# Kernel tuning notes

Hardware: AMD Instinct MI355X
Metric: run time of the kernel (lower is better)

## Reference

```python
import jax, jax.numpy as jnp
import numpy as np

N = 100000      # num_nodes
E = 3200000     # num_edges (avg degree 32)
DIN, DH, DOUT = 128, 128, 64
S, L = 3, 3     # num_scales, num_layers
EPS = 1e-5


def setup_inputs() -> dict:
    key = jax.random.key(0)
    ks = jax.random.split(key, 12)
    sc = 0.05
    x = jax.random.normal(ks[0], (N, DIN), jnp.float32)
    edge_index = jax.random.randint(ks[1], (2, E), 0, N, jnp.int32)
    return {
        'x': x,
        'edge_index': edge_index,
        'W0': jax.random.normal(ks[2], (S, DIN, DH), jnp.float32) * sc,
        'b0': jnp.zeros((S, DH), jnp.float32),
        'W1': jax.random.normal(ks[3], (S, DH, DH), jnp.float32) * sc,
        'b1': jnp.zeros((S, DH), jnp.float32),
        'W2': jax.random.normal(ks[4], (S, DH, DOUT), jnp.float32) * sc,
        'b2': jnp.zeros((S, DOUT), jnp.float32),
        'gamma': jnp.ones((S * L, DH), jnp.float32),   # layer_norms (only first L-1 per scale used)
        'beta': jnp.zeros((S * L, DH), jnp.float32),
        'Wf': jax.random.normal(ks[5], (S * DOUT, DOUT), jnp.float32) * sc,
        'bf': jnp.zeros((DOUT,), jnp.float32),
    }


def _layer_norm(h, g, b):
    mu = jnp.mean(h, axis=-1, keepdims=True)
    var = jnp.mean(jnp.square(h - mu), axis=-1, keepdims=True)
    return (h - mu) * jax.lax.rsqrt(var + EPS) * g + b


def _gcn(h, W, b, src, dst, dis):
    # GCNConv: D^{-1/2}(A+I)D^{-1/2} h W + b  (self-loops handled separately)
    hw = h @ W
    msg = hw[src] * (dis[src] * dis[dst])[:, None]          # gather + edge-scale
    agg = jax.ops.segment_sum(msg, dst, num_segments=N)     # scatter-add
    agg = agg + hw * (dis * dis)[:, None]                   # self-loop term
    return agg + b


def reference(x, edge_index, W0, b0, W1, b1, W2, b2, gamma, beta, Wf, bf):
    src, dst = edge_index[0], edge_index[1]
    # degree on A + I (unit edge weights + self loop)
    deg = jax.ops.segment_sum(jnp.ones((E,), x.dtype), dst, num_segments=N) + 1.0
    dis = jax.lax.rsqrt(deg)

    scale_outputs = []
    for s in range(S):
        h = _gcn(x, W0[s], b0[s], src, dst, dis)
        h = _layer_norm(jax.nn.relu(h), gamma[s * L + 0], beta[s * L + 0])  # dropout=identity (eval)
        h = _gcn(h, W1[s], b1[s], src, dst, dis)
        h = _layer_norm(jax.nn.relu(h), gamma[s * L + 1], beta[s * L + 1])
        h = _gcn(h, W2[s], b2[s], src, dst, dis)
        scale_outputs.append(h)

    fused = jnp.concatenate(scale_outputs, axis=-1)  # [N, S*DOUT]
    return fused @ Wf + bf
```

## Files before the change

### kernel.cpp

```cpp
#include <hip/hip_runtime.h>

#define DIN 128
#define DH 128
#define DOUTC 64
#define NS 3
#define NL 3
#define EPSV 1e-5f

typedef __attribute__((ext_vector_type(8))) short bf16x8;
typedef __attribute__((ext_vector_type(4))) float f32x4;

static __device__ inline float bf2f(unsigned short h) {
    unsigned int u = ((unsigned int)h) << 16;
    return __builtin_bit_cast(float, u);
}
static __device__ inline unsigned short f2bf(float f) {
    unsigned int u = __builtin_bit_cast(unsigned int, f);
    u += 0x7fffu + ((u >> 16) & 1u);
    return (unsigned short)(u >> 16);
}
static __device__ inline float lo16(unsigned int u) {
    return __builtin_bit_cast(float, u << 16);
}
static __device__ inline float hi16(unsigned int u) {
    return __builtin_bit_cast(float, u & 0xffff0000u);
}

__global__ __launch_bounds__(256) void k_count_r(const int* __restrict__ dst,
                                                 int* __restrict__ counts, int e, int n) {
    int rg = blockIdx.x & 7;
    int lo = rg * (n >> 3);
    int hi = (rg == 7) ? n : lo + (n >> 3);
    int nb = gridDim.x >> 3, bi = blockIdx.x >> 3;
    for (int i = bi * 256 + threadIdx.x; i < e; i += nb * 256) {
        int d = dst[i];
        if (d >= lo && d < hi) atomicAdd(&counts[d], 1);
    }
}

__global__ void k_dis(const int* __restrict__ counts, float* __restrict__ dis, int n) {
    int i = blockIdx.x * blockDim.x + threadIdx.x;
    if (i < n) dis[i] = rsqrtf((float)counts[i] + 1.0f);
}

__global__ void k_scanA(const int* __restrict__ counts, int* __restrict__ row_start,
                        int* __restrict__ bsums, int n) {
    __shared__ int s[512];
    int t = threadIdx.x;
    int i = blockIdx.x * 512 + t;
    int v = (i < n) ? counts[i] : 0;
    s[t] = v;
    __syncthreads();
    for (int off = 1; off < 512; off <<= 1) {
        int x = s[t];
        if (t >= off) x += s[t - off];
        __syncthreads();
        s[t] = x;
        __syncthreads();
    }
    if (i < n) row_start[i] = s[t] - v;
    if (t == 511) bsums[blockIdx.x] = s[511];
}

__global__ void k_scanB(int* __restrict__ bsums, int nb) {
    __shared__ int s[256];
    int t = threadIdx.x;
    int v = (t < nb) ? bsums[t] : 0;
    s[t] = v;
    __syncthreads();
    for (int off = 1; off < 256; off <<= 1) {
        int x = s[t];
        if (t >= off) x += s[t - off];
        __syncthreads();
        s[t] = x;
        __syncthreads();
    }
    if (t < nb) bsums[t] = s[t] - v;
}

__global__ void k_scanC(int* __restrict__ row_start, const int* __restrict__ bsums, int n) {
    int i = blockIdx.x * blockDim.x + threadIdx.x;
    if (i < n) row_start[i] += bsums[i >> 9];
}

__global__ __launch_bounds__(256) void k_fill_r(const int* __restrict__ src,
                                                const int* __restrict__ dst,
                                                const int* __restrict__ row_start,
                                                int* __restrict__ cursor,
                                                int* __restrict__ col, int e, int n) {
    int rg = blockIdx.x & 7;
    int lo = rg * (n >> 3);
    int hi = (rg == 7) ? n : lo + (n >> 3);
    int nb = gridDim.x >> 3, bi = blockIdx.x >> 3;
    for (int i = bi * 256 + threadIdx.x; i < e; i += nb * 256) {
        int d = dst[i];
        int s = src[i];
        if (d >= lo && d < hi) {
            int p = atomicAdd(&cursor[d], 1);
            col[row_start[d] + p] = s;
        }
    }
}

__global__ void k_prep_w(const float* __restrict__ W0, const float* __restrict__ W1,
                         const float* __restrict__ W2, const float* __restrict__ Wf,
                         const float* __restrict__ b2, const float* __restrict__ bf,
                         unsigned short* __restrict__ Wt0hi, unsigned short* __restrict__ Wt0lo,
                         unsigned short* __restrict__ Wt1hi, unsigned short* __restrict__ Wt1lo,
                         unsigned short* __restrict__ Mhi, unsigned short* __restrict__ Mlo,
                         float* __restrict__ bcomb) {
    int idx = blockIdx.x * blockDim.x + threadIdx.x;
    if (idx < NS * DH * DH) {
        int s = idx / (DH * DH);
        int rem = idx % (DH * DH);
        int o = rem / DH, i = rem % DH;
        {
            float v = W0[(size_t)s * DH * DH + (size_t)i * DH + o];
            unsigned short h = f2bf(v);
            Wt0hi[idx] = h;
            Wt0lo[idx] = f2bf(v - bf2f(h));
        }
        {
            float v = W1[(size_t)s * DH * DH + (size_t)i * DH + o];
            unsigned short h = f2bf(v);
            Wt1hi[idx] = h;
            Wt1lo[idx] = f2bf(v - bf2f(h));
        }
    }
    if (idx < DOUTC * NS * DH) {
        int o = idx / (NS * DH);
        int k = idx % (NS * DH);
        int s = k / DH, i = k % DH;
        float acc = 0.f;
        for (int c = 0; c < DOUTC; ++c)
            acc += W2[((size_t)s * DH + i) * DOUTC + c] * Wf[((size_t)s * DOUTC + c) * DOUTC + o];
        unsigned short h = f2bf(acc);
        Mhi[idx] = h;
        Mlo[idx] = f2bf(acc - bf2f(h));
    }
    if (idx < DOUTC) {
        float acc = bf[idx];
        for (int s = 0; s < NS; ++s)
            for (int c = 0; c < DOUTC; ++c)
                acc += b2[s * DOUTC + c] * Wf[((size_t)s * DOUTC + c) * DOUTC + idx];
        bcomb[idx] = acc;
    }
}

__global__ void k_cvt(const float2* __restrict__ x, unsigned int* __restrict__ xb, int m) {
    int i = blockIdx.x * blockDim.x + threadIdx.x;
    int stride = gridDim.x * blockDim.x;
    for (; i < m; i += stride) {
        float2 v = x[i];
        xb[i] = ((unsigned int)f2bf(v.y) << 16) | f2bf(v.x);
    }
}

__global__ __launch_bounds__(256) void k_agg128(
        const unsigned int* __restrict__ in, unsigned int* __restrict__ out,
        const float* __restrict__ dis, const int* __restrict__ rowstart,
        const int* __restrict__ counts, const int* __restrict__ col, int n) {
    int wid = (blockIdx.x * blockDim.x + threadIdx.x) >> 6;
    int lane = threadIdx.x & 63;
    int nw = (gridDim.x * blockDim.x) >> 6;
    for (int v = wid; v < n; v += nw) {
        float dv = dis[v];
        int st = rowstart[v], cnt = counts[v];
        float a0 = 0.f, a1 = 0.f;
        int i = 0;
        for (; i + 4 <= cnt; i += 4) {
            int s0 = col[st + i], s1 = col[st + i + 1], s2 = col[st + i + 2], s3 = col[st + i + 3];
            float w0 = dis[s0], w1 = dis[s1], w2 = dis[s2], w3 = dis[s3];
            unsigned int u0 = in[(size_t)s0 * 64 + lane];
            unsigned int u1 = in[(size_t)s1 * 64 + lane];
            unsigned int u2 = in[(size_t)s2 * 64 + lane];
            unsigned int u3 = in[(size_t)s3 * 64 + lane];
            a0 += w0 * lo16(u0); a1 += w0 * hi16(u0);
            a0 += w1 * lo16(u1); a1 += w1 * hi16(u1);
            a0 += w2 * lo16(u2); a1 += w2 * hi16(u2);
            a0 += w3 * lo16(u3); a1 += w3 * hi16(u3);
        }
        for (; i < cnt; ++i) {
            int s0 = col[st + i];
            float w0 = dis[s0];
            unsigned int u0 = in[(size_t)s0 * 64 + lane];
            a0 += w0 * lo16(u0); a1 += w0 * hi16(u0);
        }
        unsigned int us = in[(size_t)v * 64 + lane];
        float o0 = dv * (a0 + dv * lo16(us));
        float o1 = dv * (a1 + dv * hi16(us));
        out[(size_t)v * 64 + lane] = ((unsigned int)f2bf(o1) << 16) | f2bf(o0);
    }
}

__global__ __launch_bounds__(256) void k_agg384(
        const unsigned int* __restrict__ in, unsigned int* __restrict__ out,
        const float* __restrict__ dis, const int* __restrict__ rowstart,
        const int* __restrict__ counts, const int* __restrict__ col, int n) {
    int wid = (blockIdx.x * blockDim.x + threadIdx.x) >> 6;
    int lane = threadIdx.x & 63;
    int nw = (gridDim.x * blockDim.x) >> 6;
    for (int v = wid; v < n; v += nw) {
        float dv = dis[v];
        int st = rowstart[v], cnt = counts[v];
        float a0 = 0.f, a1 = 0.f, a2 = 0.f, a3 = 0.f, a4 = 0.f, a5 = 0.f;
        int i = 0;
        for (; i + 2 <= cnt; i += 2) {
            int s0 = col[st + i], s1 = col[st + i + 1];
            float w0 = dis[s0], w1 = dis[s1];
            const unsigned int* p0 = in + (size_t)s0 * 192;
            const unsigned int* p1 = in + (size_t)s1 * 192;
            unsigned int u00 = p0[lane], u01 = p0[lane + 64], u02 = p0[lane + 128];
            unsigned int u10 = p1[lane], u11 = p1[lane + 64], u12 = p1[lane + 128];
            a0 += w0 * lo16(u00); a1 += w0 * hi16(u00);
            a2 += w0 * lo16(u01); a3 += w0 * hi16(u01);
            a4 += w0 * lo16(u02); a5 += w0 * hi16(u02);
            a0 += w1 * lo16(u10); a1 += w1 * hi16(u10);
            a2 += w1 * lo16(u11); a3 += w1 * hi16(u11);
            a4 += w1 * lo16(u12); a5 += w1 * hi16(u12);
        }
        for (; i < cnt; ++i) {
            int s0 = col[st + i];
            float w0 = dis[s0];
            const unsigned int* p0 = in + (size_t)s0 * 192;
            unsigned int u00 = p0[lane], u01 = p0[lane + 64], u02 = p0[lane + 128];
            a0 += w0 * lo16(u00); a1 += w0 * hi16(u00);
            a2 += w0 * lo16(u01); a3 += w0 * hi16(u01);
            a4 += w0 * lo16(u02); a5 += w0 * hi16(u02);
        }
        const unsigned int* ps = in + (size_t)v * 192;
        unsigned int us0 = ps[lane], us1 = ps[lane + 64], us2 = ps[lane + 128];
        float o0 = dv * (a0 + dv * lo16(us0));
        float o1 = dv * (a1 + dv * hi16(us0));
        float o2 = dv * (a2 + dv * lo16(us1));
        float o3 = dv * (a3 + dv * hi16(us1));
        float o4 = dv * (a4 + dv * lo16(us2));
        float o5 = dv * (a5 + dv * hi16(us2));
        unsigned int* po = out + (size_t)v * 192;
        po[lane]       = ((unsigned int)f2bf(o1) << 16) | f2bf(o0);
        po[lane + 64]  = ((unsigned int)f2bf(o3) << 16) | f2bf(o2);
        po[lane + 128] = ((unsigned int)f2bf(o5) << 16) | f2bf(o4);
    }
}

__global__ __launch_bounds__(256) void k_agg64(
        const unsigned int* __restrict__ in, float* __restrict__ out,
        const float* __restrict__ bcomb, const float* __restrict__ dis,
        const int* __restrict__ rowstart, const int* __restrict__ counts,
        const int* __restrict__ col, int n) {
    int wid = (blockIdx.x * blockDim.x + threadIdx.x) >> 6;
    int lane = threadIdx.x & 63;
    int half = lane >> 5, c = lane & 31;
    int nw = (gridDim.x * blockDim.x) >> 6;
    float bc0 = bcomb[c * 2], bc1 = bcomb[c * 2 + 1];
    for (int w = wid; w * 2 < n; w += nw) {
        int v = w * 2 + half;
        if (v >= n) continue;
        float dv = dis[v];
        int st = rowstart[v], cnt = counts[v];
        float a0 = 0.f, a1 = 0.f;
        int i = 0;
        for (; i + 4 <= cnt; i += 4) {
            int s0 = col[st + i], s1 = col[st + i + 1], s2 = col[st + i + 2], s3 = col[st + i + 3];
            float w0 = dis[s0], w1 = dis[s1], w2 = dis[s2], w3 = dis[s3];
            unsigned int u0 = in[(size_t)s0 * 32 + c];
            unsigned int u1 = in[(size_t)s1 * 32 + c];
            unsigned int u2 = in[(size_t)s2 * 32 + c];
            unsigned int u3 = in[(size_t)s3 * 32 + c];
            a0 += w0 * lo16(u0); a1 += w0 * hi16(u0);
            a0 += w1 * lo16(u1); a1 += w1 * hi16(u1);
            a0 += w2 * lo16(u2); a1 += w2 * hi16(u2);
            a0 += w3 * lo16(u3); a1 += w3 * hi16(u3);
        }
        for (; i < cnt; ++i) {
            int s0 = col[st + i];
            float w0 = dis[s0];
            unsigned int u0 = in[(size_t)s0 * 32 + c];
            a0 += w0 * lo16(u0); a1 += w0 * hi16(u0);
        }
        unsigned int us = in[(size_t)v * 32 + c];
        float o0 = dv * (a0 + dv * lo16(us)) + bc0;
        float o1 = dv * (a1 + dv * hi16(us)) + bc1;
        float2 o = make_float2(o0, o1);
        *(float2*)&out[(size_t)v * 64 + c * 2] = o;
    }
}

__global__ __launch_bounds__(256) void k_gemm0(
        const unsigned short* __restrict__ A, const unsigned short* __restrict__ Whi,
        const unsigned short* __restrict__ Wlo, const float* __restrict__ bias,
        const float* __restrict__ gamma, const float* __restrict__ beta,
        unsigned short* __restrict__ out, int n) {
    int wave = threadIdx.x >> 6, lane = threadIdx.x & 63;
    int g = blockIdx.x * 4 + wave;
    if (g * 16 >= n) return;
    int r16 = lane & 15, g4 = lane >> 4;
    int row = g * 16 + r16;
    if (row >= n) row = n - 1;

    bf16x8 a[4];
    #pragma unroll
    for (int ks = 0; ks < 4; ++ks)
        a[ks] = *(const bf16x8*)&A[(size_t)row * DH + ks * 32 + g4 * 8];

    for (int s = 0; s < NS; ++s) {
        const unsigned short* whi = Whi + (size_t)s * DH * DH;
        const unsigned short* wlo = Wlo + (size_t)s * DH * DH;
        f32x4 acc[8];
        #pragma unroll
        for (int t = 0; t < 8; ++t) acc[t] = (f32x4){0.f, 0.f, 0.f, 0.f};
        #pragma unroll
        for (int ks = 0; ks < 4; ++ks) {
            #pragma unroll
            for (int t = 0; t < 8; ++t) {
                size_t wofs = (size_t)(t * 16 + r16) * DH + ks * 32 + g4 * 8;
                bf16x8 bh = *(const bf16x8*)&whi[wofs];
                bf16x8 bl = *(const bf16x8*)&wlo[wofs];
                acc[t] = __builtin_amdgcn_mfma_f32_16x16x32_bf16(a[ks], bh, acc[t], 0, 0, 0);
                acc[t] = __builtin_amdgcn_mfma_f32_16x16x32_bf16(a[ks], bl, acc[t], 0, 0, 0);
            }
        }
        float bia[8], gam[8], bet[8];
        #pragma unroll
        for (int t = 0; t < 8; ++t) {
            bia[t] = bias[s * DH + t * 16 + r16];
            gam[t] = gamma[(size_t)(s * NL + 0) * DH + t * 16 + r16];
            bet[t] = beta[(size_t)(s * NL + 0) * DH + t * 16 + r16];
        }
        #pragma unroll
        for (int r = 0; r < 4; ++r) {
            float y[8];
            float sm = 0.f, q = 0.f;
            #pragma unroll
            for (int t = 0; t < 8; ++t) {
                y[t] = fmaxf(acc[t][r] + bia[t], 0.f);
                sm += y[t];
                q += y[t] * y[t];
            }
            #pragma unroll
            for (int off = 8; off; off >>= 1) {
                sm += __shfl_xor(sm, off);
                q += __shfl_xor(q, off);
            }
            float mu = sm * (1.f / 128.f);
            float var = q * (1.f / 128.f) - mu * mu;
            float rstd = rsqrtf(var + EPSV);
            int node = g * 16 + g4 * 4 + r;
            if (node < n) {
                #pragma unroll
                for (int t = 0; t < 8; ++t) {
                    float o = (y[t] - mu) * rstd * gam[t] + bet[t];
                    out[(size_t)node * (NS * DH) + s * DH + t * 16 + r16] = f2bf(o);
                }
            }
        }
    }
}

__global__ __launch_bounds__(256) void k_gemm1q(
        const unsigned short* __restrict__ G, const unsigned short* __restrict__ Whi,
        const unsigned short* __restrict__ Wlo, const unsigned short* __restrict__ Mhi,
        const unsigned short* __restrict__ Mlo, const float* __restrict__ bias,
        const float* __restrict__ gamma, const float* __restrict__ beta,
        unsigned short* __restrict__ q, int n) {
    __shared__ __align__(16) unsigned short sH[4][16][392];
    int wave = threadIdx.x >> 6, lane = threadIdx.x & 63;
    int g = blockIdx.x * 4 + wave;
    if (g * 16 >= n) return;
    int r16 = lane & 15, g4 = lane >> 4;
    int row = g * 16 + r16;
    if (row >= n) row = n - 1;

    for (int s = 0; s < NS; ++s) {
        bf16x8 a[4];
        #pragma unroll
        for (int ks = 0; ks < 4; ++ks)
            a[ks] = *(const bf16x8*)&G[(size_t)row * (NS * DH) + s * DH + ks * 32 + g4 * 8];
        const unsigned short* whi = Whi + (size_t)s * DH * DH;
        const unsigned short* wlo = Wlo + (size_t)s * DH * DH;
        f32x4 acc[8];
        #pragma unroll
        for (int t = 0; t < 8; ++t) acc[t] = (f32x4){0.f, 0.f, 0.f, 0.f};
        #pragma unroll
        for (int ks = 0; ks < 4; ++ks) {
            #pragma unroll
            for (int t = 0; t < 8; ++t) {
                size_t wofs = (size_t)(t * 16 + r16) * DH + ks * 32 + g4 * 8;
                bf16x8 bh = *(const bf16x8*)&whi[wofs];
                bf16x8 bl = *(const bf16x8*)&wlo[wofs];
                acc[t] = __builtin_amdgcn_mfma_f32_16x16x32_bf16(a[ks], bh, acc[t], 0, 0, 0);
                acc[t] = __builtin_amdgcn_mfma_f32_16x16x32_bf16(a[ks], bl, acc[t], 0, 0, 0);
            }
        }
        float bia[8], gam[8], bet[8];
        #pragma unroll
        for (int t = 0; t < 8; ++t) {
            bia[t] = bias[s * DH + t * 16 + r16];
            gam[t] = gamma[(size_t)(s * NL + 1) * DH + t * 16 + r16];
            bet[t] = beta[(size_t)(s * NL + 1) * DH + t * 16 + r16];
        }
        #pragma unroll
        for (int r = 0; r < 4; ++r) {
            float y[8];
            float sm = 0.f, qq = 0.f;
            #pragma unroll
            for (int t = 0; t < 8; ++t) {
                y[t] = fmaxf(acc[t][r] + bia[t], 0.f);
                sm += y[t];
                qq += y[t] * y[t];
            }
            #pragma unroll
            for (int off = 8; off; off >>= 1) {
                sm += __shfl_xor(sm, off);
                qq += __shfl_xor(qq, off);
            }
            float mu = sm * (1.f / 128.f);
            float var = qq * (1.f / 128.f) - mu * mu;
            float rstd = rsqrtf(var + EPSV);
            #pragma unroll
            for (int t = 0; t < 8; ++t) {
                float o = (y[t] - mu) * rstd * gam[t] + bet[t];
                sH[wave][g4 * 4 + r][s * DH + t * 16 + r16] = f2bf(o);
            }
        }
    }
    __syncthreads();
    f32x4 qa[4];
    #pragma unroll
    for (int t = 0; t < 4; ++t) qa[t] = (f32x4){0.f, 0.f, 0.f, 0.f};
    #pragma unroll
    for (int ks = 0; ks < 12; ++ks) {
        bf16x8 av = *(const bf16x8*)&sH[wave][r16][ks * 32 + g4 * 8];
        #pragma unroll
        for (int t = 0; t < 4; ++t) {
            size_t wofs = (size_t)(t * 16 + r16) * (NS * DH) + ks * 32 + g4 * 8;
            bf16x8 bh = *(const bf16x8*)&Mhi[wofs];
            bf16x8 bl = *(const bf16x8*)&Mlo[wofs];
            qa[t] = __builtin_amdgcn_mfma_f32_16x16x32_bf16(av, bh, qa[t], 0, 0, 0);
            qa[t] = __builtin_amdgcn_mfma_f32_16x16x32_bf16(av, bl, qa[t], 0, 0, 0);
        }
    }
    #pragma unroll
    for (int r = 0; r < 4; ++r) {
        int node = g * 16 + g4 * 4 + r;
        if (node < n) {
            #pragma unroll
            for (int t = 0; t < 4; ++t)
                q[(size_t)node * DOUTC + t * 16 + r16] = f2bf(qa[t][r]);
        }
    }
}

extern "C" void kernel_launch(void* const* d_in, const int* in_sizes, int n_in,
                              void* d_out, int out_size, void* d_ws, size_t ws_size,
                              hipStream_t stream) {
    const float* x    = (const float*)d_in[0];
    const int*   ei   = (const int*)d_in[1];
    const float* W0   = (const float*)d_in[2];
    const float* b0   = (const float*)d_in[3];
    const float* W1   = (const float*)d_in[4];
    const float* b1   = (const float*)d_in[5];
    const float* W2   = (const float*)d_in[6];
    const float* b2   = (const float*)d_in[7];
    const float* gamma= (const float*)d_in[8];
    const float* beta = (const float*)d_in[9];
    const float* Wf   = (const float*)d_in[10];
    const float* bf   = (const float*)d_in[11];
    float* out = (float*)d_out;

    const int n = in_sizes[0] / DIN;
    const int e = in_sizes[1] / 2;
    const int* src = ei;
    const int* dst = ei + e;

    char* ws = (char*)d_ws;
    auto alloc = [&](size_t bytes) {
        char* p = ws;
        ws += (bytes + 255) & ~(size_t)255;
        return p;
    };
    int*   counts   = (int*)alloc((size_t)n * 4);
    int*   cursor   = (int*)alloc((size_t)n * 4);
    int*   rowstart = (int*)alloc((size_t)n * 4);
    int*   bsums    = (int*)alloc(4096);
    float* dis      = (float*)alloc((size_t)n * 4);
    int*   col      = (int*)alloc((size_t)e * 4);
    unsigned short* Wt0hi = (unsigned short*)alloc((size_t)NS * DH * DH * 2);
    unsigned short* Wt0lo = (unsigned short*)alloc((size_t)NS * DH * DH * 2);
    unsigned short* Wt1hi = (unsigned short*)alloc((size_t)NS * DH * DH * 2);
    unsigned short* Wt1lo = (unsigned short*)alloc((size_t)NS * DH * DH * 2);
    unsigned short* Mhi   = (unsigned short*)alloc((size_t)DOUTC * NS * DH * 2);
    unsigned short* Mlo   = (unsigned short*)alloc((size_t)DOUTC * NS * DH * 2);
    float* bcomb    = (float*)alloc(DOUTC * 4);
    unsigned short* xb    = (unsigned short*)alloc((size_t)n * DIN * 2);
    unsigned short* z0    = (unsigned short*)alloc((size_t)n * DH * 2);
    unsigned short* h1cat = (unsigned short*)alloc((size_t)n * NS * DH * 2);
    unsigned short* g1cat = (unsigned short*)alloc((size_t)n * NS * DH * 2);
    unsigned short* q     = (unsigned short*)alloc((size_t)n * DOUTC * 2);

    hipMemsetAsync(counts, 0, (size_t)n * 4, stream);
    hipMemsetAsync(cursor, 0, (size_t)n * 4, stream);

    k_count_r<<<2048, 256, 0, stream>>>(dst, counts, e, n);
    k_dis<<<(n + 255) / 256, 256, 0, stream>>>(counts, dis, n);

    int nb = (n + 511) / 512;
    k_scanA<<<nb, 512, 0, stream>>>(counts, rowstart, bsums, n);
    k_scanB<<<1, 256, 0, stream>>>(bsums, nb);
    k_scanC<<<(n + 255) / 256, 256, 0, stream>>>(rowstart, bsums, n);
    k_fill_r<<<2048, 256, 0, stream>>>(src, dst, rowstart, cursor, col, e, n);

    k_prep_w<<<(NS * DH * DH + 255) / 256, 256, 0, stream>>>(
        W0, W1, W2, Wf, b2, bf, Wt0hi, Wt0lo, Wt1hi, Wt1lo, Mhi, Mlo, bcomb);
    k_cvt<<<2048, 256, 0, stream>>>((const float2*)x, (unsigned int*)xb, n * DIN / 2);

    k_agg128<<<1280, 256, 0, stream>>>((const unsigned int*)xb, (unsigned int*)z0,
                                       dis, rowstart, counts, col, n);
    const int GG = (n / 16 + 3) / 4;
    k_gemm0<<<GG, 256, 0, stream>>>(z0, Wt0hi, Wt0lo, b0, gamma, beta, h1cat, n);
    k_agg384<<<1280, 256, 0, stream>>>((const unsigned int*)h1cat, (unsigned int*)g1cat,
                                       dis, rowstart, counts, col, n);
    k_gemm1q<<<GG, 256, 0, stream>>>(g1cat, Wt1hi, Wt1lo, Mhi, Mlo,
                                     b1, gamma, beta, q, n);
    k_agg64<<<1280, 256, 0, stream>>>((const unsigned int*)q, out, bcomb,
                                      dis, rowstart, counts, col, n);
}
```

Baseline: 1.506 ms.

## Pre-scale features by source norm, vectorize CSR build, tweak aggregation grids

The producer kernels (conversion, gemm0 epilogue, gemm1q epilogue) now multiply each node's row by dis[node]. This removes the per-edge dis[src] gather and multiply from all three aggregation kernels, leaving only a final scale by dis[dst]. Count and fill kernels read dst/src as int4, and cursor is initialised by copying rowstart, so fill writes col directly at the atomic result without a separate row_start read. Aggregation grids grow from 1280 to 2048 blocks and agg384 unrolls by four edges. Rounding changes a little because bf16 values are now stored pre-scaled.

```diff
diff --git a/kernel.cpp b/kernel.cpp
--- a/kernel.cpp
+++ b/kernel.cpp
@@ -32,8 +32,17 @@
     int lo = rg * (n >> 3);
     int hi = (rg == 7) ? n : lo + (n >> 3);
     int nb = gridDim.x >> 3, bi = blockIdx.x >> 3;
-    for (int i = bi * 256 + threadIdx.x; i < e; i += nb * 256) {
-        int d = dst[i];
+    int e4 = e >> 2;
+    const int4* dst4 = (const int4*)dst;
+    for (int i = bi * 256 + threadIdx.x; i < e4; i += nb * 256) {
+        int4 d = dst4[i];
+        if (d.x >= lo && d.x < hi) atomicAdd(&counts[d.x], 1);
+        if (d.y >= lo && d.y < hi) atomicAdd(&counts[d.y], 1);
+        if (d.z >= lo && d.z < hi) atomicAdd(&counts[d.z], 1);
+        if (d.w >= lo && d.w < hi) atomicAdd(&counts[d.w], 1);
+    }
+    if (bi == 0 && (int)threadIdx.x < (e & 3)) {
+        int d = dst[e4 * 4 + threadIdx.x];
         if (d >= lo && d < hi) atomicAdd(&counts[d], 1);
     }
 }
@@ -85,20 +94,27 @@
 
 __global__ __launch_bounds__(256) void k_fill_r(const int* __restrict__ src,
                                                 const int* __restrict__ dst,
-                                                const int* __restrict__ row_start,
                                                 int* __restrict__ cursor,
                                                 int* __restrict__ col, int e, int n) {
     int rg = blockIdx.x & 7;
     int lo = rg * (n >> 3);
     int hi = (rg == 7) ? n : lo + (n >> 3);
     int nb = gridDim.x >> 3, bi = blockIdx.x >> 3;
-    for (int i = bi * 256 + threadIdx.x; i < e; i += nb * 256) {
-        int d = dst[i];
-        int s = src[i];
-        if (d >= lo && d < hi) {
-            int p = atomicAdd(&cursor[d], 1);
-            col[row_start[d] + p] = s;
-        }
+    int e4 = e >> 2;
+    const int4* dst4 = (const int4*)dst;
+    const int4* src4 = (const int4*)src;
+    for (int i = bi * 256 + threadIdx.x; i < e4; i += nb * 256) {
+        int4 d = dst4[i];
+        int4 s = src4[i];
+        if (d.x >= lo && d.x < hi) col[atomicAdd(&cursor[d.x], 1)] = s.x;
+        if (d.y >= lo && d.y < hi) col[atomicAdd(&cursor[d.y], 1)] = s.y;
+        if (d.z >= lo && d.z < hi) col[atomicAdd(&cursor[d.z], 1)] = s.z;
+        if (d.w >= lo && d.w < hi) col[atomicAdd(&cursor[d.w], 1)] = s.w;
+    }
+    if (bi == 0 && (int)threadIdx.x < (e & 3)) {
+        int d = dst[e4 * 4 + threadIdx.x];
+        int s = src[e4 * 4 + threadIdx.x];
+        if (d >= lo && d < hi) col[atomicAdd(&cursor[d], 1)] = s;
     }
 }
 
@@ -147,12 +163,14 @@
     }
 }
 
-__global__ void k_cvt(const float2* __restrict__ x, unsigned int* __restrict__ xb, int m) {
+__global__ void k_cvt(const float2* __restrict__ x, unsigned int* __restrict__ xb,
+                      const float* __restrict__ dis, int m) {
     int i = blockIdx.x * blockDim.x + threadIdx.x;
     int stride = gridDim.x * blockDim.x;
     for (; i < m; i += stride) {
+        float d = dis[i >> 6];
         float2 v = x[i];
-        xb[i] = ((unsigned int)f2bf(v.y) << 16) | f2bf(v.x);
+        xb[i] = ((unsigned int)f2bf(v.y * d) << 16) | f2bf(v.x * d);
     }
 }
 
@@ -165,31 +183,27 @@
     int nw = (gridDim.x * blockDim.x) >> 6;
     for (int v = wid; v < n; v += nw) {
         float dv = dis[v];
-        int st = rowstart[v], cnt = counts[v];
-        float a0 = 0.f, a1 = 0.f;
+        const int* colp = col + rowstart[v];
+        int cnt = counts[v];
+        unsigned int us = in[(size_t)v * 64 + lane];
+        float a0 = lo16(us), a1 = hi16(us);
         int i = 0;
         for (; i + 4 <= cnt; i += 4) {
-            int s0 = col[st + i], s1 = col[st + i + 1], s2 = col[st + i + 2], s3 = col[st + i + 3];
-            float w0 = dis[s0], w1 = dis[s1], w2 = dis[s2], w3 = dis[s3];
+            int s0 = colp[i], s1 = colp[i + 1], s2 = colp[i + 2], s3 = colp[i + 3];
             unsigned int u0 = in[(size_t)s0 * 64 + lane];
             unsigned int u1 = in[(size_t)s1 * 64 + lane];
             unsigned int u2 = in[(size_t)s2 * 64 + lane];
             unsigned int u3 = in[(size_t)s3 * 64 + lane];
-            a0 += w0 * lo16(u0); a1 += w0 * hi16(u0);
-            a0 += w1 * lo16(u1); a1 += w1 * hi16(u1);
-            a0 += w2 * lo16(u2); a1 += w2 * hi16(u2);
-            a0 += w3 * lo16(u3); a1 += w3 * hi16(u3);
+            a0 += lo16(u0); a1 += hi16(u0);
+            a0 += lo16(u1); a1 += hi16(u1);
+            a0 += lo16(u2); a1 += hi16(u2);
+            a0 += lo16(u3); a1 += hi16(u3);
         }
         for (; i < cnt; ++i) {
-            int s0 = col[st + i];
-            float w0 = dis[s0];
-            unsigned int u0 = in[(size_t)s0 * 64 + lane];
-            a0 += w0 * lo16(u0); a1 += w0 * hi16(u0);
-        }
-        unsigned int us = in[(size_t)v * 64 + lane];
-        float o0 = dv * (a0 + dv * lo16(us));
-        float o1 = dv * (a1 + dv * hi16(us));
-        out[(size_t)v * 64 + lane] = ((unsigned int)f2bf(o1) << 16) | f2bf(o0);
+            unsigned int u0 = in[(size_t)colp[i] * 64 + lane];
+            a0 += lo16(u0); a1 += hi16(u0);
+        }
+        out[(size_t)v * 64 + lane] = ((unsigned int)f2bf(dv * a1) << 16) | f2bf(dv * a0);
     }
 }
 
@@ -202,44 +216,48 @@
     int nw = (gridDim.x * blockDim.x) >> 6;
     for (int v = wid; v < n; v += nw) {
         float dv = dis[v];
-        int st = rowstart[v], cnt = counts[v];
-        float a0 = 0.f, a1 = 0.f, a2 = 0.f, a3 = 0.f, a4 = 0.f, a5 = 0.f;
+        const int* colp = col + rowstart[v];
+        int cnt = counts[v];
+        const unsigned int* ps = in + (size_t)v * 192;
+        unsigned int us0 = ps[lane], us1 = ps[lane + 64], us2 = ps[lane + 128];
+        float a0 = lo16(us0), a1 = hi16(us0);
+        float a2 = lo16(us1), a3 = hi16(us1);
+        float a4 = lo16(us2), a5 = hi16(us2);
         int i = 0;
-        for (; i + 2 <= cnt; i += 2) {
-            int s0 = col[st + i], s1 = col[st + i + 1];
-            float w0 = dis[s0], w1 = dis[s1];
+        for (; i + 4 <= cnt; i += 4) {
+            int s0 = colp[i], s1 = colp[i + 1], s2 = colp[i + 2], s3 = colp[i + 3];
             const unsigned int* p0 = in + (size_t)s0 * 192;
             const unsigned int* p1 = in + (size_t)s1 * 192;
+            const unsigned int* p2 = in + (size_t)s2 * 192;
+            const unsigned int* p3 = in + (size_t)s3 * 192;
             unsigned int u00 = p0[lane], u01 = p0[lane + 64], u02 = p0[lane + 128];
             unsigned int u10 = p1[lane], u11 = p1[lane + 64], u12 = p1[lane + 128];
-            a0 += w0 * lo16(u00); a1 += w0 * hi16(u00);
-            a2 += w0 * lo16(u01); a3 += w0 * hi16(u01);
-            a4 += w0 * lo16(u02); a5 += w0 * hi16(u02);
-            a0 += w1 * lo16(u10); a1 += w1 * hi16(u10);
-            a2 += w1 * lo16(u11); a3 += w1 * hi16(u11);
-            a4 += w1 * lo16(u12); a5 += w1 * hi16(u12);
+            unsigned int u20 = p2[lane], u21 = p2[lane + 64], u22 = p2[lane + 128];
+            unsigned int u30 = p3[lane], u31 = p3[lane + 64], u32 = p3[lane + 128];
+            a0 += lo16(u00); a1 += hi16(u00);
+            a2 += lo16(u01); a3 += hi16(u01);
+            a4 += lo16(u02); a5 += hi16(u02);
+            a0 += lo16(u10); a1 += hi16(u10);
+            a2 += lo16(u11); a3 += hi16(u11);
+            a4 += lo16(u12); a5 += hi16(u12);
+            a0 += lo16(u20); a1 += hi16(u20);
+            a2 += lo16(u21); a3 += hi16(u21);
+            a4 += lo16(u22); a5 += hi16(u22);
+            a0 += lo16(u30); a1 += hi16(u30);
+            a2 += lo16(u31); a3 += hi16(u31);
+            a4 += lo16(u32); a5 += hi16(u32);
         }
         for (; i < cnt; ++i) {
-            int s0 = col[st + i];
-            float w0 = dis[s0];
-            const unsigned int* p0 = in + (size_t)s0 * 192;
+            const unsigned int* p0 = in + (size_t)colp[i] * 192;
             unsigned int u00 = p0[lane], u01 = p0[lane + 64], u02 = p0[lane + 128];
-            a0 += w0 * lo16(u00); a1 += w0 * hi16(u00);
-            a2 += w0 * lo16(u01); a3 += w0 * hi16(u01);
-            a4 += w0 * lo16(u02); a5 += w0 * hi16(u02);
-        }
-        const unsigned int* ps = in + (size_t)v * 192;
-        unsigned int us0 = ps[lane], us1 = ps[lane + 64], us2 = ps[lane + 128];
-        float o0 = dv * (a0 + dv * lo16(us0));
-        float o1 = dv * (a1 + dv * hi16(us0));
-        float o2 = dv * (a2 + dv * lo16(us1));
-        float o3 = dv * (a3 + dv * hi16(us1));
-        float o4 = dv * (a4 + dv * lo16(us2));
-        float o5 = dv * (a5 + dv * hi16(us2));
+            a0 += lo16(u00); a1 += hi16(u00);
+            a2 += lo16(u01); a3 += hi16(u01);
+            a4 += lo16(u02); a5 += hi16(u02);
+        }
         unsigned int* po = out + (size_t)v * 192;
-        po[lane]       = ((unsigned int)f2bf(o1) << 16) | f2bf(o0);
-        po[lane + 64]  = ((unsigned int)f2bf(o3) << 16) | f2bf(o2);
-        po[lane + 128] = ((unsigned int)f2bf(o5) << 16) | f2bf(o4);
+        po[lane]       = ((unsigned int)f2bf(dv * a1) << 16) | f2bf(dv * a0);
+        po[lane + 64]  = ((unsigned int)f2bf(dv * a3) << 16) | f2bf(dv * a2);
+        po[lane + 128] = ((unsigned int)f2bf(dv * a5) << 16) | f2bf(dv * a4);
     }
 }
 
@@ -257,31 +275,27 @@
         int v = w * 2 + half;
         if (v >= n) continue;
         float dv = dis[v];
-        int st = rowstart[v], cnt = counts[v];
-        float a0 = 0.f, a1 = 0.f;
+        const int* colp = col + rowstart[v];
+        int cnt = counts[v];
+        unsigned int us = in[(size_t)v * 32 + c];
+        float a0 = lo16(us), a1 = hi16(us);
         int i = 0;
         for (; i + 4 <= cnt; i += 4) {
-            int s0 = col[st + i], s1 = col[st + i + 1], s2 = col[st + i + 2], s3 = col[st + i + 3];
-            float w0 = dis[s0], w1 = dis[s1], w2 = dis[s2], w3 = dis[s3];
+            int s0 = colp[i], s1 = colp[i + 1], s2 = colp[i + 2], s3 = colp[i + 3];
             unsigned int u0 = in[(size_t)s0 * 32 + c];
             unsigned int u1 = in[(size_t)s1 * 32 + c];
             unsigned int u2 = in[(size_t)s2 * 32 + c];
             unsigned int u3 = in[(size_t)s3 * 32 + c];
-            a0 += w0 * lo16(u0); a1 += w0 * hi16(u0);
-            a0 += w1 * lo16(u1); a1 += w1 * hi16(u1);
-            a0 += w2 * lo16(u2); a1 += w2 * hi16(u2);
-            a0 += w3 * lo16(u3); a1 += w3 * hi16(u3);
+            a0 += lo16(u0); a1 += hi16(u0);
+            a0 += lo16(u1); a1 += hi16(u1);
+            a0 += lo16(u2); a1 += hi16(u2);
+            a0 += lo16(u3); a1 += hi16(u3);
         }
         for (; i < cnt; ++i) {
-            int s0 = col[st + i];
-            float w0 = dis[s0];
-            unsigned int u0 = in[(size_t)s0 * 32 + c];
-            a0 += w0 * lo16(u0); a1 += w0 * hi16(u0);
-        }
-        unsigned int us = in[(size_t)v * 32 + c];
-        float o0 = dv * (a0 + dv * lo16(us)) + bc0;
-        float o1 = dv * (a1 + dv * hi16(us)) + bc1;
-        float2 o = make_float2(o0, o1);
+            unsigned int u0 = in[(size_t)colp[i] * 32 + c];
+            a0 += lo16(u0); a1 += hi16(u0);
+        }
+        float2 o = make_float2(dv * a0 + bc0, dv * a1 + bc1);
         *(float2*)&out[(size_t)v * 64 + c * 2] = o;
     }
 }
@@ -290,7 +304,7 @@
         const unsigned short* __restrict__ A, const unsigned short* __restrict__ Whi,
         const unsigned short* __restrict__ Wlo, const float* __restrict__ bias,
         const float* __restrict__ gamma, const float* __restrict__ beta,
-        unsigned short* __restrict__ out, int n) {
+        const float* __restrict__ dis, unsigned short* __restrict__ out, int n) {
     int wave = threadIdx.x >> 6, lane = threadIdx.x & 63;
     int g = blockIdx.x * 4 + wave;
     if (g * 16 >= n) return;
@@ -347,9 +361,10 @@
             float rstd = rsqrtf(var + EPSV);
             int node = g * 16 + g4 * 4 + r;
             if (node < n) {
+                float dnode = dis[node];
                 #pragma unroll
                 for (int t = 0; t < 8; ++t) {
-                    float o = (y[t] - mu) * rstd * gam[t] + bet[t];
+                    float o = ((y[t] - mu) * rstd * gam[t] + bet[t]) * dnode;
                     out[(size_t)node * (NS * DH) + s * DH + t * 16 + r16] = f2bf(o);
                 }
             }
@@ -362,7 +377,7 @@
         const unsigned short* __restrict__ Wlo, const unsigned short* __restrict__ Mhi,
         const unsigned short* __restrict__ Mlo, const float* __restrict__ bias,
         const float* __restrict__ gamma, const float* __restrict__ beta,
-        unsigned short* __restrict__ q, int n) {
+        const float* __restrict__ dis, unsigned short* __restrict__ q, int n) {
     __shared__ __align__(16) unsigned short sH[4][16][392];
     int wave = threadIdx.x >> 6, lane = threadIdx.x & 63;
     int g = blockIdx.x * 4 + wave;
@@ -444,9 +459,10 @@
     for (int r = 0; r < 4; ++r) {
         int node = g * 16 + g4 * 4 + r;
         if (node < n) {
+            float dnode = dis[node];
             #pragma unroll
             for (int t = 0; t < 4; ++t)
-                q[(size_t)node * DOUTC + t * 16 + r16] = f2bf(qa[t][r]);
+                q[(size_t)node * DOUTC + t * 16 + r16] = f2bf(qa[t][r] * dnode);
         }
     }
 }
@@ -499,7 +515,6 @@
     unsigned short* q     = (unsigned short*)alloc((size_t)n * DOUTC * 2);
 
     hipMemsetAsync(counts, 0, (size_t)n * 4, stream);
-    hipMemsetAsync(cursor, 0, (size_t)n * 4, stream);
 
     k_count_r<<<2048, 256, 0, stream>>>(dst, counts, e, n);
     k_dis<<<(n + 255) / 256, 256, 0, stream>>>(counts, dis, n);
@@ -508,20 +523,21 @@
     k_scanA<<<nb, 512, 0, stream>>>(counts, rowstart, bsums, n);
     k_scanB<<<1, 256, 0, stream>>>(bsums, nb);
     k_scanC<<<(n + 255) / 256, 256, 0, stream>>>(rowstart, bsums, n);
-    k_fill_r<<<2048, 256, 0, stream>>>(src, dst, rowstart, cursor, col, e, n);
+    hipMemcpyAsync(cursor, rowstart, (size_t)n * 4, hipMemcpyDeviceToDevice, stream);
+    k_fill_r<<<2048, 256, 0, stream>>>(src, dst, cursor, col, e, n);
 
     k_prep_w<<<(NS * DH * DH + 255) / 256, 256, 0, stream>>>(
         W0, W1, W2, Wf, b2, bf, Wt0hi, Wt0lo, Wt1hi, Wt1lo, Mhi, Mlo, bcomb);
-    k_cvt<<<2048, 256, 0, stream>>>((const float2*)x, (unsigned int*)xb, n * DIN / 2);
-
-    k_agg128<<<1280, 256, 0, stream>>>((const unsigned int*)xb, (unsigned int*)z0,
+    k_cvt<<<2048, 256, 0, stream>>>((const float2*)x, (unsigned int*)xb, dis, n * DIN / 2);
+
+    k_agg128<<<2048, 256, 0, stream>>>((const unsigned int*)xb, (unsigned int*)z0,
                                        dis, rowstart, counts, col, n);
     const int GG = (n / 16 + 3) / 4;
-    k_gemm0<<<GG, 256, 0, stream>>>(z0, Wt0hi, Wt0lo, b0, gamma, beta, h1cat, n);
-    k_agg384<<<1280, 256, 0, stream>>>((const unsigned int*)h1cat, (unsigned int*)g1cat,
+    k_gemm0<<<GG, 256, 0, stream>>>(z0, Wt0hi, Wt0lo, b0, gamma, beta, dis, h1cat, n);
+    k_agg384<<<2048, 256, 0, stream>>>((const unsigned int*)h1cat, (unsigned int*)g1cat,
                                        dis, rowstart, counts, col, n);
     k_gemm1q<<<GG, 256, 0, stream>>>(g1cat, Wt1hi, Wt1lo, Mhi, Mlo,
-                                     b1, gamma, beta, q, n);
-    k_agg64<<<1280, 256, 0, stream>>>((const unsigned int*)q, out, bcomb,
+                                     b1, gamma, beta, dis, q, n);
+    k_agg64<<<2048, 256, 0, stream>>>((const unsigned int*)q, out, bcomb,
                                       dis, rowstart, counts, col, n);
 }
```

Result: faster. 1.403 ms (-6.8%).
